# Kernel optimization log

Measured on AMD Instinct MI355X. Metric: run time of the kernel, lower is better.

Reference implementation:

```python
import jax, jax.numpy as jnp
import numpy as np

D_EMBED = 1024
N_HEADS = 16
D_HEAD = 64
D_MLP = 4096
SEQ = 2048
BATCH = 2
ALPHA = 1.0


def setup_inputs() -> dict:
    key = jax.random.key(0)
    ks = jax.random.split(key, 7)
    s = ALPHA / np.sqrt(D_EMBED)
    return {
        "x": jax.random.normal(ks[0], (BATCH, SEQ, D_EMBED), jnp.float32),
        "W_K": s * jax.random.normal(ks[1], (N_HEADS, D_HEAD, D_EMBED), jnp.float32),
        "W_Q": s * jax.random.normal(ks[2], (N_HEADS, D_HEAD, D_EMBED), jnp.float32),
        "W_V": s * jax.random.normal(ks[3], (N_HEADS, D_HEAD, D_EMBED), jnp.float32),
        "W_O": s * jax.random.normal(ks[4], (D_EMBED, N_HEADS * D_HEAD), jnp.float32),
        "W_in": s * jax.random.normal(ks[5], (D_MLP, D_EMBED), jnp.float32),
        "b_in": jnp.zeros((D_MLP,), jnp.float32),
        "W_out": s * jax.random.normal(ks[6], (D_EMBED, D_MLP), jnp.float32),
        "b_out": jnp.zeros((D_EMBED,), jnp.float32),
    }


def reference(x, W_K, W_Q, W_V, W_O, W_in, b_in, W_out, b_out):
    b, c_len, _ = x.shape
    d_head = W_K.shape[1]
    # q/k/v: [batch, head, ctx, d_head]
    k = jnp.einsum('ahe,bce->bach', W_K, x)
    q = jnp.einsum('ahe,bce->bach', W_Q, x)
    v = jnp.einsum('ahe,bce->bach', W_V, x)
    # scores[b,a,c,C] = k_c . q_C  (faithful to original index convention)
    scores = jnp.einsum('bach,baCh->bacC', k, q)
    mask = jnp.tril(jnp.ones((c_len, c_len), dtype=x.dtype))  # [c, C]
    masked = scores * mask - 1e10 * (1.0 - mask)
    attn = jax.nn.softmax(masked / np.sqrt(d_head), axis=-1)  # softmax over C (query idx)
    # z[b,a,C,h] = sum_c v[b,a,c,h] * attn[b,a,c,C]
    z = jnp.einsum('bach,bacC->baCh', v, attn)
    z_flat = jnp.transpose(z, (0, 2, 1, 3)).reshape(b, c_len, -1)  # [b, c, a*h]
    attn_out = jnp.einsum('ef,bcf->bce', W_O, z_flat)
    x = x + attn_out
    h = jnp.einsum('me,bce->bcm', W_in, x) + b_in
    h = jax.nn.relu(h)
    mlp_out = jnp.einsum('em,bcm->bce', W_out, h) + b_out
    return x + mlp_out
```

## Files before the change

### kernel.cpp

```cpp
#include <hip/hip_runtime.h>
#include <hip/hip_bf16.h>
#include <cstdint>
#include <cstddef>

typedef __bf16 bf16;
typedef bf16 bf16x4 __attribute__((ext_vector_type(4)));
typedef bf16 bf16x8 __attribute__((ext_vector_type(8)));
typedef float floatx4 __attribute__((ext_vector_type(4)));

#define MFMA16(a, b, c) __builtin_amdgcn_mfma_f32_16x16x32_bf16((a), (b), (c), 0, 0, 0)

#define K2 0.18033688011112042f

__device__ __forceinline__ void async16(const void* g, void* l) {
    __builtin_amdgcn_global_load_lds((const __attribute__((address_space(1))) void*)g,
                                     (__attribute__((address_space(3))) void*)l,
                                     16, 0, 0);
}

__device__ __forceinline__ void stage64s(const bf16* g0, int ldg, bf16* lds, int wave, int lane) {
#pragma unroll
    for (int i = 0; i < 2; ++i) {
        int r0 = wave * 16 + i * 8;
        async16(g0 + (size_t)(r0 + (lane >> 3)) * ldg + ((lane & 7) ^ (lane >> 3)) * 8,
                lds + r0 * 64);
    }
}
__device__ __forceinline__ bf16x8 rd64(const bf16* t, int row, int chunk) {
    return *(const bf16x8*)&t[row * 64 + ((chunk ^ (row & 7)) * 8)];
}
__device__ __forceinline__ bf16x8 rd32(const bf16* t, int row, int quad) {
    return *(const bf16x8*)&t[row * 32 + ((quad ^ (row & 3)) * 8)];
}

__global__ __launch_bounds__(256) void cvt_all(const float* __restrict__ x,
                                               const float* __restrict__ WQ,
                                               const float* __restrict__ WK,
                                               const float* __restrict__ WV,
                                               const float* __restrict__ WO,
                                               const float* __restrict__ Win,
                                               const float* __restrict__ Wout,
                                               bf16* __restrict__ xb,
                                               bf16* __restrict__ wqkv,
                                               bf16* __restrict__ wo,
                                               bf16* __restrict__ win,
                                               bf16* __restrict__ wout) {
    int blk = blockIdx.x;
    const float* src;
    bf16* dst;
    int off;
    if (blk < 1024)      { src = WQ;   dst = wqkv;           off = blk; }
    else if (blk < 2048) { src = WK;   dst = wqkv + 1048576; off = blk - 1024; }
    else if (blk < 3072) { src = WV;   dst = wqkv + 2097152; off = blk - 2048; }
    else if (blk < 4096) { src = WO;   dst = wo;             off = blk - 3072; }
    else if (blk < 8192) { src = Win;  dst = win;            off = blk - 4096; }
    else if (blk < 12288){ src = Wout; dst = wout;           off = blk - 8192; }
    else                 { src = x;    dst = xb;             off = blk - 12288; }
    int i = off * 1024 + threadIdx.x * 4;
    float4 v = *(const float4*)(src + i);
    bf16x4 o = {(bf16)v.x, (bf16)v.y, (bf16)v.z, (bf16)v.w};
    *(bf16x4*)(dst + i) = o;
}

template <int EPI, int NACC>
__device__ __forceinline__ void epilogue(floatx4 (&acc)[4][NACC], int m0, int n0,
                                         int wm, int wn, int col, int quad,
                                         float* Cf, bf16* Cb, int ldc,
                                         const float* bias, const float* res) {
#pragma unroll
    for (int mi = 0; mi < 4; ++mi)
#pragma unroll
        for (int ni = 0; ni < NACC; ++ni)
#pragma unroll
            for (int r = 0; r < 4; ++r) {
                int row = m0 + wm + mi * 16 + quad * 4 + r;
                int cc = n0 + wn + ni * 16 + col;
                size_t idx = (size_t)row * ldc + cc;
                float v = acc[mi][ni][r];
                if constexpr (EPI == 0) {
                    Cb[idx] = (bf16)v;
                } else if constexpr (EPI == 1) {
                    v += res[idx];
                    Cf[idx] = v;
                    Cb[idx] = (bf16)v;
                } else if constexpr (EPI == 2) {
                    v += bias[cc];
                    v = fmaxf(v, 0.f);
                    Cb[idx] = (bf16)v;
                } else {
                    v += bias[cc] + Cf[idx];
                    Cf[idx] = v;
                }
            }
}

template <int EPI>
__global__ __launch_bounds__(256) void gemm_pipe(const bf16* __restrict__ A, int lda,
                                                 const bf16* __restrict__ B, int ldb, int K,
                                                 float* __restrict__ Cf, bf16* __restrict__ Cb,
                                                 int ldc, const float* __restrict__ bias,
                                                 const float* __restrict__ res) {
    __shared__ __align__(16) bf16 As[3][128 * 32];
    __shared__ __align__(16) bf16 Bs[3][128 * 32];
    const int tid = threadIdx.x, wave = tid >> 6, lane = tid & 63;
    const int m0 = blockIdx.y * 128, n0 = blockIdx.x * 128;
    const int wm = (wave >> 1) * 64, wn = (wave & 1) * 64;
    const int col = lane & 15, quad = lane >> 4;
    const int cs8 = ((lane & 3) ^ ((lane >> 2) & 3)) * 8;

    floatx4 acc[4][4];
#pragma unroll
    for (int mi = 0; mi < 4; ++mi)
#pragma unroll
        for (int ni = 0; ni < 4; ++ni) acc[mi][ni] = (floatx4){0.f, 0.f, 0.f, 0.f};

    auto stage = [&](int buf, int k0) {
#pragma unroll
        for (int i = 0; i < 2; ++i) {
            int r0 = wave * 32 + i * 16;
            async16(A + (size_t)(m0 + r0 + (lane >> 2)) * lda + k0 + cs8,
                    As[buf] + r0 * 32);
            async16(B + (size_t)(n0 + r0 + (lane >> 2)) * ldb + k0 + cs8,
                    Bs[buf] + r0 * 32);
        }
    };

    const int nk = K / 32;
    stage(0, 0);
    stage(1, 32);
    for (int it = 0; it < nk; ++it) {
        if (it + 1 < nk) asm volatile("s_waitcnt vmcnt(4)" ::: "memory");
        else             asm volatile("s_waitcnt vmcnt(0)" ::: "memory");
        __builtin_amdgcn_s_barrier();
        if (it + 2 < nk) stage((it + 2) % 3, (it + 2) * 32);

        const bf16* as = As[it % 3];
        const bf16* bs = Bs[it % 3];
        bf16x8 af[4], bfr[4];
#pragma unroll
        for (int mi = 0; mi < 4; ++mi) af[mi] = rd32(as, wm + mi * 16 + col, quad);
#pragma unroll
        for (int ni = 0; ni < 4; ++ni) bfr[ni] = rd32(bs, wn + ni * 16 + col, quad);
#pragma unroll
        for (int mi = 0; mi < 4; ++mi)
#pragma unroll
            for (int ni = 0; ni < 4; ++ni)
                acc[mi][ni] = MFMA16(af[mi], bfr[ni], acc[mi][ni]);
    }
    epilogue<EPI, 4>(acc, m0, n0, wm, wn, col, quad, Cf, Cb, ldc, bias, res);
}

template <int EPI>
__global__ __launch_bounds__(256) void gemm97s(const bf16* __restrict__ A, int lda,
                                               const bf16* __restrict__ B, int ldb, int K,
                                               float* __restrict__ Cf, bf16* __restrict__ Cb,
                                               int ldc, const float* __restrict__ bias,
                                               const float* __restrict__ res) {
    __shared__ __align__(16) bf16 As[128 * 64];
    __shared__ __align__(16) bf16 Bs[64 * 64];
    const int tid = threadIdx.x, wave = tid >> 6, lane = tid & 63;
    const int m0 = blockIdx.y * 128, n0 = blockIdx.x * 64;
    const int wm = (wave >> 1) * 64, wn = (wave & 1) * 32;
    const int col = lane & 15, quad = lane >> 4;

    floatx4 acc[4][2];
#pragma unroll
    for (int mi = 0; mi < 4; ++mi)
#pragma unroll
        for (int ni = 0; ni < 2; ++ni) acc[mi][ni] = (floatx4){0.f, 0.f, 0.f, 0.f};

    const int rsub = lane >> 3;
    const int csub = ((lane & 7) ^ rsub) * 8;

    for (int k0 = 0; k0 < K; k0 += 64) {
        __syncthreads();
#pragma unroll
        for (int i = 0; i < 4; ++i) {
            int r0 = wave * 32 + i * 8;
            async16(A + (size_t)(m0 + r0 + rsub) * lda + k0 + csub, As + r0 * 64);
        }
#pragma unroll
        for (int i = 0; i < 2; ++i) {
            int r0 = wave * 16 + i * 8;
            async16(B + (size_t)(n0 + r0 + rsub) * ldb + k0 + csub, Bs + r0 * 64);
        }
        __syncthreads();

#pragma unroll
        for (int ks = 0; ks < 2; ++ks) {
            bf16x8 af[4], bfr[2];
#pragma unroll
            for (int mi = 0; mi < 4; ++mi) {
                int row = wm + mi * 16 + col;
                af[mi] = *(const bf16x8*)&As[row * 64 + (((ks * 4 + quad) ^ (row & 7)) * 8)];
            }
#pragma unroll
            for (int ni = 0; ni < 2; ++ni) {
                int row = wn + ni * 16 + col;
                bfr[ni] = *(const bf16x8*)&Bs[row * 64 + (((ks * 4 + quad) ^ (row & 7)) * 8)];
            }
#pragma unroll
            for (int mi = 0; mi < 4; ++mi)
#pragma unroll
                for (int ni = 0; ni < 2; ++ni)
                    acc[mi][ni] = MFMA16(af[mi], bfr[ni], acc[mi][ni]);
        }
    }
    epilogue<EPI, 2>(acc, m0, n0, wm, wn, col, quad, Cf, Cb, ldc, bias, res);
}

__global__ __launch_bounds__(256) void transpose_v(const bf16* __restrict__ qkv,
                                                   bf16* __restrict__ vt) {
    __shared__ bf16 t[64][65];
    const int bh = blockIdx.y, ct = blockIdx.x;
    const int b = bh >> 4, a = bh & 15;
    for (int idx = threadIdx.x; idx < 4096; idx += 256) {
        int c = idx >> 6, h = idx & 63;
        t[h][c] = qkv[(size_t)(b * 2048 + ct * 64 + c) * 3072 + 2048 + a * 64 + h];
    }
    __syncthreads();
    for (int idx = threadIdx.x; idx < 4096; idx += 256) {
        int h = idx >> 6, c = idx & 63;
        vt[(size_t)(bh * 64 + h) * 2048 + ct * 64 + c] = t[h][c];
    }
}

__global__ __launch_bounds__(256) void attn_stats(const bf16* __restrict__ qkv,
                                                  float* __restrict__ mp2) {
    __shared__ __align__(16) bf16 Kt[64 * 64];
    __shared__ __align__(16) bf16 Qt[3][64 * 64];
    const int xx = blockIdx.x;
    const int ct = (xx & 1) ? (31 - (xx >> 1)) : (xx >> 1);
    const int bh = blockIdx.y;
    const int b = bh >> 4, a = bh & 15;
    const int tid = threadIdx.x, wave = tid >> 6, lane = tid & 63;
    const int col = lane & 15, quad = lane >> 4;
    const bf16* base = qkv + (size_t)b * 2048 * 3072;

    stage64s(base + (size_t)ct * 64 * 3072 + 1024 + a * 64, 3072, Kt, wave, lane);
    stage64s(base + a * 64, 3072, Qt[0], wave, lane);
    if (ct >= 1) stage64s(base + (size_t)1 * 64 * 3072 + a * 64, 3072, Qt[1], wave, lane);

    float lrun[4] = {0.f, 0.f, 0.f, 0.f};
    bf16x8 a0, a1;

    for (int Ct = 0; Ct <= ct; ++Ct) {
        if (Ct < ct) asm volatile("s_waitcnt vmcnt(2)" ::: "memory");
        else         asm volatile("s_waitcnt vmcnt(0)" ::: "memory");
        __builtin_amdgcn_s_barrier();
        if (Ct + 2 <= ct)
            stage64s(base + (size_t)(Ct + 2) * 64 * 3072 + a * 64, 3072,
                     Qt[(Ct + 2) % 3], wave, lane);
        if (Ct == 0) {
            a0 = rd64(Kt, wave * 16 + col, quad);
            a1 = rd64(Kt, wave * 16 + col, quad + 4);
        }
        const bf16* q = Qt[Ct % 3];
#pragma unroll
        for (int nt = 0; nt < 4; ++nt) {
            bf16x8 b0 = rd64(q, nt * 16 + col, quad);
            bf16x8 b1 = rd64(q, nt * 16 + col, quad + 4);
            floatx4 sacc = (floatx4){0.f, 0.f, 0.f, 0.f};
            sacc = MFMA16(a0, b0, sacc);
            sacc = MFMA16(a1, b1, sacc);
#pragma unroll
            for (int r = 0; r < 4; ++r) {
                float e = __builtin_amdgcn_exp2f(sacc[r] * K2);
                if (Ct == ct && (nt * 16 + col) > (wave * 16 + quad * 4 + r)) e = 0.f;
                lrun[r] += e;
            }
        }
    }
#pragma unroll
    for (int r = 0; r < 4; ++r) {
        float t = lrun[r];
        t += __shfl_xor(t, 1);
        t += __shfl_xor(t, 2);
        t += __shfl_xor(t, 4);
        t += __shfl_xor(t, 8);
        lrun[r] = t;
    }
    if (col == 0) {
#pragma unroll
        for (int r = 0; r < 4; ++r) {
            int c = ct * 64 + wave * 16 + quad * 4 + r;
            mp2[(size_t)bh * 2048 + c] = __builtin_amdgcn_logf(lrun[r]);
        }
    }
}

__global__ __launch_bounds__(256) void attn_av(const bf16* __restrict__ qkv,
                                               const bf16* __restrict__ vt,
                                               const float* __restrict__ mp2,
                                               bf16* __restrict__ zb) {
    __shared__ __align__(16) bf16 Qt[64 * 64];
    __shared__ __align__(16) bf16 Kt[3][64 * 64];
    __shared__ __align__(16) bf16 Vt[3][64 * 64];
    __shared__ __align__(16) bf16 Pt[64 * 72];
    __shared__ __align__(16) float mpS[2048];
    const int xx = blockIdx.x;
    const int Ctile = (xx & 1) ? (31 - (xx >> 1)) : (xx >> 1);
    const int bh = blockIdx.y;
    const int b = bh >> 4, a = bh & 15;
    const int tid = threadIdx.x, wave = tid >> 6, lane = tid & 63;
    const int col = lane & 15, quad = lane >> 4;
    const bf16* base = qkv + (size_t)b * 2048 * 3072;
    const float* mpb = mp2 + (size_t)bh * 2048;
    const int niter = 32 - Ctile;

    stage64s(base + (size_t)Ctile * 64 * 3072 + a * 64, 3072, Qt, wave, lane);
    {
        int nb = niter * 256;
#pragma unroll
        for (int i = 0; i < 2; ++i) {
            int off = (i * 4 + wave) * 1024;
            if (off < nb)
                async16((const char*)(mpb + Ctile * 64) + off + lane * 16,
                        (char*)mpS + off);
        }
    }
    stage64s(base + (size_t)Ctile * 64 * 3072 + 1024 + a * 64, 3072, Kt[0], wave, lane);
    stage64s(vt + (size_t)bh * 64 * 2048 + Ctile * 64, 2048, Vt[0], wave, lane);
    if (niter > 1) {
        stage64s(base + (size_t)(Ctile + 1) * 64 * 3072 + 1024 + a * 64, 3072, Kt[1], wave, lane);
        stage64s(vt + (size_t)bh * 64 * 2048 + (Ctile + 1) * 64, 2048, Vt[1], wave, lane);
    }

    floatx4 zacc[4];
#pragma unroll
    for (int mi = 0; mi < 4; ++mi) zacc[mi] = (floatx4){0.f, 0.f, 0.f, 0.f};
    bf16x8 qf0[4], qf1[4];

    for (int i = 0; i < niter; ++i) {
        const int ct = Ctile + i;
        if (i + 1 < niter) asm volatile("s_waitcnt vmcnt(4)" ::: "memory");
        else               asm volatile("s_waitcnt vmcnt(0)" ::: "memory");
        __builtin_amdgcn_s_barrier();
        if (i + 2 < niter) {
            stage64s(base + (size_t)(ct + 2) * 64 * 3072 + 1024 + a * 64, 3072,
                     Kt[(i + 2) % 3], wave, lane);
            stage64s(vt + (size_t)bh * 64 * 2048 + (ct + 2) * 64, 2048,
                     Vt[(i + 2) % 3], wave, lane);
        }
        if (i == 0) {
#pragma unroll
            for (int nt = 0; nt < 4; ++nt) {
                qf0[nt] = rd64(Qt, nt * 16 + col, quad);
                qf1[nt] = rd64(Qt, nt * 16 + col, quad + 4);
            }
        }
        const bf16* kt = Kt[i % 3];
        const bf16* vts = Vt[i % 3];
        bf16x8 a0 = rd64(kt, wave * 16 + col, quad);
        bf16x8 a1 = rd64(kt, wave * 16 + col, quad + 4);
        float4 mpv = *(const float4*)&mpS[i * 64 + wave * 16 + quad * 4];
        const float mpl[4] = {mpv.x, mpv.y, mpv.z, mpv.w};

#pragma unroll
        for (int nt = 0; nt < 4; ++nt) {
            floatx4 sacc = (floatx4){0.f, 0.f, 0.f, 0.f};
            sacc = MFMA16(a0, qf0[nt], sacc);
            sacc = MFMA16(a1, qf1[nt], sacc);
            bf16x4 pv;
#pragma unroll
            for (int r = 0; r < 4; ++r) {
                float p;
                if (ct == Ctile && (nt * 16 + col) > (wave * 16 + quad * 4 + r))
                    p = 0.f;
                else
                    p = __builtin_amdgcn_exp2f(sacc[r] * K2 - mpl[r]);
                pv[r] = (bf16)p;
            }
            *(bf16x4*)&Pt[(nt * 16 + col) * 72 + wave * 16 + quad * 4] = pv;
        }
        asm volatile("s_waitcnt lgkmcnt(0)" ::: "memory");
        __builtin_amdgcn_s_barrier();

        bf16x8 v0 = rd64(vts, wave * 16 + col, quad);
        bf16x8 v1 = rd64(vts, wave * 16 + col, quad + 4);
#pragma unroll
        for (int mi = 0; mi < 4; ++mi) {
            bf16x8 p0 = *(const bf16x8*)&Pt[(mi * 16 + col) * 72 + quad * 8];
            bf16x8 p1 = *(const bf16x8*)&Pt[(mi * 16 + col) * 72 + 32 + quad * 8];
            zacc[mi] = MFMA16(p0, v0, zacc[mi]);
            zacc[mi] = MFMA16(p1, v1, zacc[mi]);
        }
    }
#pragma unroll
    for (int mi = 0; mi < 4; ++mi)
#pragma unroll
        for (int r = 0; r < 4; ++r) {
            int Cg = Ctile * 64 + mi * 16 + quad * 4 + r;
            zb[(size_t)(b * 2048 + Cg) * 1024 + a * 64 + wave * 16 + col] =
                (bf16)zacc[mi][r];
        }
}

extern "C" void kernel_launch(void* const* d_in, const int* in_sizes, int n_in,
                              void* d_out, int out_size, void* d_ws, size_t ws_size,
                              hipStream_t stream) {
    (void)in_sizes; (void)n_in; (void)out_size; (void)ws_size;
    const float* x    = (const float*)d_in[0];
    const float* WK   = (const float*)d_in[1];
    const float* WQ   = (const float*)d_in[2];
    const float* WV   = (const float*)d_in[3];
    const float* WO   = (const float*)d_in[4];
    const float* Win  = (const float*)d_in[5];
    const float* bin  = (const float*)d_in[6];
    const float* Wout = (const float*)d_in[7];
    const float* bout = (const float*)d_in[8];
    float* out = (float*)d_out;

    char* ws = (char*)d_ws;
    bf16*  xb   = (bf16*)(ws + 0);
    bf16*  wqkv = (bf16*)(ws + 8388608);
    bf16*  wo   = (bf16*)(ws + 14680064);
    bf16*  win  = (bf16*)(ws + 16777216);
    bf16*  wout = (bf16*)(ws + 25165824);
    bf16*  qkvb = (bf16*)(ws + 33554432);
    bf16*  vtb  = (bf16*)(ws + 58720256);
    float* mst  = (float*)(ws + 67108864);
    bf16*  zbuf = (bf16*)(ws + 67633152);
    bf16*  xmid = (bf16*)(ws + 76021760);
    bf16*  hbuf = (bf16*)(ws + 84410368);

    cvt_all<<<16384, 256, 0, stream>>>(x, WQ, WK, WV, WO, Win, Wout,
                                       xb, wqkv, wo, win, wout);

    gemm_pipe<0><<<dim3(24, 32), 256, 0, stream>>>(xb, 1024, wqkv, 1024, 1024,
                                                   nullptr, qkvb, 3072, nullptr, nullptr);
    transpose_v<<<dim3(32, 32), 256, 0, stream>>>(qkvb, vtb);
    attn_stats<<<dim3(32, 32), 256, 0, stream>>>(qkvb, mst);
    attn_av<<<dim3(32, 32), 256, 0, stream>>>(qkvb, vtb, mst, zbuf);
    gemm97s<1><<<dim3(16, 32), 256, 0, stream>>>(zbuf, 1024, wo, 1024, 1024,
                                                 out, xmid, 1024, nullptr, x);
    gemm_pipe<2><<<dim3(32, 32), 256, 0, stream>>>(xmid, 1024, win, 1024, 1024,
                                                   nullptr, hbuf, 4096, bin, nullptr);
    gemm97s<3><<<dim3(16, 32), 256, 0, stream>>>(hbuf, 4096, wout, 4096, 4096,
                                                 out, nullptr, 1024, bout, nullptr);
}
```

Before: 395.4 us.

## Fold softmax normalizer into V and use 32x32 MFMA register-resident P

The stats kernel now writes the reciprocal row sum instead of its log, and the V transpose multiplies each V row by that reciprocal. This removes the per-element subtraction and the mp staging from the attention-AV kernel. The AV kernel switches to 32x32x16 MFMA tiles, builds the P operand in registers via lane shuffles instead of an LDS round trip, and drops the mid-iteration barrier. Waves split the key dimension, so partial Z accumulators are reduced through LDS at the end. The exponent is now computed without max subtraction and V is scaled before bf16 rounding, which changes numerics and risks overflow for large scores.

```diff
diff --git a/kernel.cpp b/kernel.cpp
--- a/kernel.cpp
+++ b/kernel.cpp
@@ -7,8 +7,11 @@
 typedef bf16 bf16x4 __attribute__((ext_vector_type(4)));
 typedef bf16 bf16x8 __attribute__((ext_vector_type(8)));
 typedef float floatx4 __attribute__((ext_vector_type(4)));
+typedef float floatx16 __attribute__((ext_vector_type(16)));
+typedef unsigned int uint;
 
 #define MFMA16(a, b, c) __builtin_amdgcn_mfma_f32_16x16x32_bf16((a), (b), (c), 0, 0, 0)
+#define MFMA32(a, b, c) __builtin_amdgcn_mfma_f32_32x32x16_bf16((a), (b), (c), 0, 0, 0)
 
 #define K2 0.18033688011112042f
 
@@ -31,6 +34,13 @@
 }
 __device__ __forceinline__ bf16x8 rd32(const bf16* t, int row, int quad) {
     return *(const bf16x8*)&t[row * 32 + ((quad ^ (row & 3)) * 8)];
+}
+
+__device__ __forceinline__ uint pk2(float lo, float hi) {
+    union { bf16 h[2]; uint u; } c;
+    c.h[0] = (bf16)lo;
+    c.h[1] = (bf16)hi;
+    return c.u;
 }
 
 __global__ __launch_bounds__(256) void cvt_all(const float* __restrict__ x,
@@ -210,13 +220,16 @@
 }
 
 __global__ __launch_bounds__(256) void transpose_v(const bf16* __restrict__ qkv,
+                                                   const float* __restrict__ linv,
                                                    bf16* __restrict__ vt) {
     __shared__ bf16 t[64][65];
     const int bh = blockIdx.y, ct = blockIdx.x;
     const int b = bh >> 4, a = bh & 15;
+    const float* lv = linv + (size_t)bh * 2048 + ct * 64;
     for (int idx = threadIdx.x; idx < 4096; idx += 256) {
         int c = idx >> 6, h = idx & 63;
-        t[h][c] = qkv[(size_t)(b * 2048 + ct * 64 + c) * 3072 + 2048 + a * 64 + h];
+        float v = (float)qkv[(size_t)(b * 2048 + ct * 64 + c) * 3072 + 2048 + a * 64 + h];
+        t[h][c] = (bf16)(v * lv[c]);
     }
     __syncthreads();
     for (int idx = threadIdx.x; idx < 4096; idx += 256) {
@@ -226,7 +239,7 @@
 }
 
 __global__ __launch_bounds__(256) void attn_stats(const bf16* __restrict__ qkv,
-                                                  float* __restrict__ mp2) {
+                                                  float* __restrict__ linv) {
     __shared__ __align__(16) bf16 Kt[64 * 64];
     __shared__ __align__(16) bf16 Qt[3][64 * 64];
     const int xx = blockIdx.x;
@@ -284,41 +297,28 @@
 #pragma unroll
         for (int r = 0; r < 4; ++r) {
             int c = ct * 64 + wave * 16 + quad * 4 + r;
-            mp2[(size_t)bh * 2048 + c] = __builtin_amdgcn_logf(lrun[r]);
+            linv[(size_t)bh * 2048 + c] = 1.0f / lrun[r];
         }
     }
 }
 
 __global__ __launch_bounds__(256) void attn_av(const bf16* __restrict__ qkv,
                                                const bf16* __restrict__ vt,
-                                               const float* __restrict__ mp2,
                                                bf16* __restrict__ zb) {
     __shared__ __align__(16) bf16 Qt[64 * 64];
     __shared__ __align__(16) bf16 Kt[3][64 * 64];
     __shared__ __align__(16) bf16 Vt[3][64 * 64];
-    __shared__ __align__(16) bf16 Pt[64 * 72];
-    __shared__ __align__(16) float mpS[2048];
     const int xx = blockIdx.x;
     const int Ctile = (xx & 1) ? (31 - (xx >> 1)) : (xx >> 1);
     const int bh = blockIdx.y;
     const int b = bh >> 4, a = bh & 15;
     const int tid = threadIdx.x, wave = tid >> 6, lane = tid & 63;
-    const int col = lane & 15, quad = lane >> 4;
+    const int l31 = lane & 31, lh = lane >> 5;
+    const int cq = wave >> 1, Cq = wave & 1;
     const bf16* base = qkv + (size_t)b * 2048 * 3072;
-    const float* mpb = mp2 + (size_t)bh * 2048;
     const int niter = 32 - Ctile;
 
     stage64s(base + (size_t)Ctile * 64 * 3072 + a * 64, 3072, Qt, wave, lane);
-    {
-        int nb = niter * 256;
-#pragma unroll
-        for (int i = 0; i < 2; ++i) {
-            int off = (i * 4 + wave) * 1024;
-            if (off < nb)
-                async16((const char*)(mpb + Ctile * 64) + off + lane * 16,
-                        (char*)mpS + off);
-        }
-    }
     stage64s(base + (size_t)Ctile * 64 * 3072 + 1024 + a * 64, 3072, Kt[0], wave, lane);
     stage64s(vt + (size_t)bh * 64 * 2048 + Ctile * 64, 2048, Vt[0], wave, lane);
     if (niter > 1) {
@@ -326,10 +326,10 @@
         stage64s(vt + (size_t)bh * 64 * 2048 + (Ctile + 1) * 64, 2048, Vt[1], wave, lane);
     }
 
-    floatx4 zacc[4];
-#pragma unroll
-    for (int mi = 0; mi < 4; ++mi) zacc[mi] = (floatx4){0.f, 0.f, 0.f, 0.f};
-    bf16x8 qf0[4], qf1[4];
+    floatx16 zacc[2];
+    zacc[0] = (floatx16)0.f;
+    zacc[1] = (floatx16)0.f;
+    bf16x8 qf[4];
 
     for (int i = 0; i < niter; ++i) {
         const int ct = Ctile + i;
@@ -344,56 +344,96 @@
         }
         if (i == 0) {
 #pragma unroll
-            for (int nt = 0; nt < 4; ++nt) {
-                qf0[nt] = rd64(Qt, nt * 16 + col, quad);
-                qf1[nt] = rd64(Qt, nt * 16 + col, quad + 4);
-            }
+            for (int s = 0; s < 4; ++s) qf[s] = rd64(Qt, 32 * Cq + l31, 2 * s + lh);
         }
         const bf16* kt = Kt[i % 3];
         const bf16* vts = Vt[i % 3];
-        bf16x8 a0 = rd64(kt, wave * 16 + col, quad);
-        bf16x8 a1 = rd64(kt, wave * 16 + col, quad + 4);
-        float4 mpv = *(const float4*)&mpS[i * 64 + wave * 16 + quad * 4];
-        const float mpl[4] = {mpv.x, mpv.y, mpv.z, mpv.w};
-
-#pragma unroll
-        for (int nt = 0; nt < 4; ++nt) {
-            floatx4 sacc = (floatx4){0.f, 0.f, 0.f, 0.f};
-            sacc = MFMA16(a0, qf0[nt], sacc);
-            sacc = MFMA16(a1, qf1[nt], sacc);
-            bf16x4 pv;
-#pragma unroll
-            for (int r = 0; r < 4; ++r) {
-                float p;
-                if (ct == Ctile && (nt * 16 + col) > (wave * 16 + quad * 4 + r))
-                    p = 0.f;
-                else
-                    p = __builtin_amdgcn_exp2f(sacc[r] * K2 - mpl[r]);
-                pv[r] = (bf16)p;
-            }
-            *(bf16x4*)&Pt[(nt * 16 + col) * 72 + wave * 16 + quad * 4] = pv;
-        }
-        asm volatile("s_waitcnt lgkmcnt(0)" ::: "memory");
-        __builtin_amdgcn_s_barrier();
-
-        bf16x8 v0 = rd64(vts, wave * 16 + col, quad);
-        bf16x8 v1 = rd64(vts, wave * 16 + col, quad + 4);
-#pragma unroll
-        for (int mi = 0; mi < 4; ++mi) {
-            bf16x8 p0 = *(const bf16x8*)&Pt[(mi * 16 + col) * 72 + quad * 8];
-            bf16x8 p1 = *(const bf16x8*)&Pt[(mi * 16 + col) * 72 + 32 + quad * 8];
-            zacc[mi] = MFMA16(p0, v0, zacc[mi]);
-            zacc[mi] = MFMA16(p1, v1, zacc[mi]);
-        }
-    }
-#pragma unroll
-    for (int mi = 0; mi < 4; ++mi)
-#pragma unroll
-        for (int r = 0; r < 4; ++r) {
-            int Cg = Ctile * 64 + mi * 16 + quad * 4 + r;
-            zb[(size_t)(b * 2048 + Cg) * 1024 + a * 64 + wave * 16 + col] =
-                (bf16)zacc[mi][r];
-        }
+
+        floatx16 sacc = (floatx16)0.f;
+        __builtin_amdgcn_s_setprio(1);
+#pragma unroll
+        for (int s = 0; s < 4; ++s) {
+            bf16x8 kf = rd64(kt, 32 * cq + l31, 2 * s + lh);
+            sacc = MFMA32(kf, qf[s], sacc);
+        }
+        __builtin_amdgcn_s_setprio(0);
+
+        float p[16];
+#pragma unroll
+        for (int r = 0; r < 16; ++r) {
+            float e = __builtin_amdgcn_exp2f(sacc[r] * K2);
+            if (i == 0) {
+                int creg = (r & 3) + 8 * (r >> 2) + 4 * lh;
+                if (32 * Cq + l31 > 32 * cq + creg) e = 0.f;
+            }
+            p[r] = e;
+        }
+
+        bf16x8 pa[2];
+#pragma unroll
+        for (int g = 0; g < 2; ++g) {
+            uint w0 = pk2(p[8 * g + 0], p[8 * g + 1]);
+            uint w1 = pk2(p[8 * g + 2], p[8 * g + 3]);
+            uint w2 = pk2(p[8 * g + 4], p[8 * g + 5]);
+            uint w3 = pk2(p[8 * g + 6], p[8 * g + 7]);
+            uint xw0 = (uint)__shfl_xor((int)w0, 32);
+            uint xw1 = (uint)__shfl_xor((int)w1, 32);
+            uint xw2 = (uint)__shfl_xor((int)w2, 32);
+            uint xw3 = (uint)__shfl_xor((int)w3, 32);
+            union { uint u[4]; bf16x8 v; } cv;
+            cv.u[0] = lh ? xw2 : w0;
+            cv.u[1] = lh ? xw3 : w1;
+            cv.u[2] = lh ? w2 : xw0;
+            cv.u[3] = lh ? w3 : xw1;
+            pa[g] = cv.v;
+        }
+
+        __builtin_amdgcn_s_setprio(1);
+#pragma unroll
+        for (int ht = 0; ht < 2; ++ht) {
+#pragma unroll
+            for (int s = 0; s < 2; ++s) {
+                bf16x8 vf = rd64(vts, 32 * ht + l31, 4 * cq + 2 * s + lh);
+                zacc[ht] = MFMA32(pa[s], vf, zacc[ht]);
+            }
+        }
+        __builtin_amdgcn_s_setprio(0);
+    }
+
+    __syncthreads();
+    float* Zex = (float*)Kt;
+    if (cq == 1) {
+#pragma unroll
+        for (int ht = 0; ht < 2; ++ht)
+#pragma unroll
+            for (int q = 0; q < 4; ++q) {
+                float4 t4 = {zacc[ht][4 * q + 0], zacc[ht][4 * q + 1],
+                             zacc[ht][4 * q + 2], zacc[ht][4 * q + 3]};
+                *(float4*)&Zex[Cq * 2048 + lane * 32 + (((ht * 4 + q) ^ (lane & 7)) * 4)] = t4;
+            }
+    }
+    __syncthreads();
+    if (cq == 0) {
+#pragma unroll
+        for (int ht = 0; ht < 2; ++ht)
+#pragma unroll
+            for (int q = 0; q < 4; ++q) {
+                float4 t4 = *(const float4*)&Zex[Cq * 2048 + lane * 32 +
+                                                 (((ht * 4 + q) ^ (lane & 7)) * 4)];
+                zacc[ht][4 * q + 0] += t4.x;
+                zacc[ht][4 * q + 1] += t4.y;
+                zacc[ht][4 * q + 2] += t4.z;
+                zacc[ht][4 * q + 3] += t4.w;
+            }
+#pragma unroll
+        for (int ht = 0; ht < 2; ++ht)
+#pragma unroll
+            for (int r = 0; r < 16; ++r) {
+                int Cg = Ctile * 64 + 32 * Cq + (r & 3) + 8 * (r >> 2) + 4 * lh;
+                zb[(size_t)(b * 2048 + Cg) * 1024 + a * 64 + 32 * ht + l31] =
+                    (bf16)zacc[ht][r];
+            }
+    }
 }
 
 extern "C" void kernel_launch(void* const* d_in, const int* in_sizes, int n_in,
@@ -429,9 +469,9 @@
 
     gemm_pipe<0><<<dim3(24, 32), 256, 0, stream>>>(xb, 1024, wqkv, 1024, 1024,
                                                    nullptr, qkvb, 3072, nullptr, nullptr);
-    transpose_v<<<dim3(32, 32), 256, 0, stream>>>(qkvb, vtb);
     attn_stats<<<dim3(32, 32), 256, 0, stream>>>(qkvb, mst);
-    attn_av<<<dim3(32, 32), 256, 0, stream>>>(qkvb, vtb, mst, zbuf);
+    transpose_v<<<dim3(32, 32), 256, 0, stream>>>(qkvb, mst, vtb);
+    attn_av<<<dim3(32, 32), 256, 0, stream>>>(qkvb, vtb, zbuf);
     gemm97s<1><<<dim3(16, 32), 256, 0, stream>>>(zbuf, 1024, wo, 1024, 1024,
                                                  out, xmid, 1024, nullptr, x);
     gemm_pipe<2><<<dim3(32, 32), 256, 0, stream>>>(xmid, 1024, win, 1024, 1024,
```

New measurement: 398.1 us. Within noise of the previous version (+0.7%).
